# Performance work log

Measured on AMD Instinct MI355X. Metric: run time of the kernel, lower is better.

## Reference

```python
import jax, jax.numpy as jnp
import numpy as np

D_MODEL = 2048
N_HEAD = 32
N_KV_HEAD = 8
N_REP = N_HEAD // N_KV_HEAD
D_K = D_MODEL // N_HEAD
THETA = 10000.0
B, S = 2, 1024


def setup_inputs() -> dict:
    key = jax.random.key(0)
    ks = jax.random.split(key, 9)
    sd = 1.0 / np.sqrt(D_MODEL)
    return {
        "x": jax.random.normal(ks[0], (B, S, D_MODEL), jnp.float32),
        "Wq": jax.random.normal(ks[1], (D_MODEL, D_MODEL), jnp.float32) * sd,
        "bq": jax.random.normal(ks[2], (D_MODEL,), jnp.float32) * 0.02,
        "Wk": jax.random.normal(ks[3], (D_MODEL, N_KV_HEAD * D_K), jnp.float32) * sd,
        "bk": jax.random.normal(ks[4], (N_KV_HEAD * D_K,), jnp.float32) * 0.02,
        "Wv": jax.random.normal(ks[5], (D_MODEL, N_KV_HEAD * D_K), jnp.float32) * sd,
        "bv": jax.random.normal(ks[6], (N_KV_HEAD * D_K,), jnp.float32) * 0.02,
        "Wo": jax.random.normal(ks[7], (D_MODEL, D_MODEL), jnp.float32) * sd,
        "bo": jax.random.normal(ks[8], (D_MODEL,), jnp.float32) * 0.02,
    }


def _apply_rope(t, pos):
    # t: [b, h, s, d_k], pos: [s]
    half = D_K // 2
    inv_freq = 1.0 / (THETA ** (jnp.arange(half, dtype=jnp.float32) * 2.0 / D_K))
    ang = pos[:, None].astype(jnp.float32) * inv_freq[None, :]  # [s, half]
    cos = jnp.cos(ang)[None, None]  # [1,1,s,half]
    sin = jnp.sin(ang)[None, None]
    te = t[..., 0::2]
    to = t[..., 1::2]
    re = te * cos - to * sin
    ro = te * sin + to * cos
    return jnp.stack([re, ro], axis=-1).reshape(t.shape)


def reference(x, Wq, bq, Wk, bk, Wv, bv, Wo, bo):
    b, s, _ = x.shape
    q = (x @ Wq + bq).reshape(b, s, N_HEAD, D_K).transpose(0, 2, 1, 3)
    k = (x @ Wk + bk).reshape(b, s, N_KV_HEAD, D_K).transpose(0, 2, 1, 3)
    v = (x @ Wv + bv).reshape(b, s, N_KV_HEAD, D_K).transpose(0, 2, 1, 3)
    pos = jnp.arange(s)
    q = _apply_rope(q, pos)
    k = _apply_rope(k, pos)
    # GQA head repeat: [b, n_kv, s, d] -> [b, n_head, s, d]
    k = jnp.repeat(k, N_REP, axis=1)
    v = jnp.repeat(v, N_REP, axis=1)
    scores = jnp.einsum('bhnd,bhmd->bhnm', q, k) / jnp.sqrt(jnp.float32(D_K))
    mask = jnp.tril(jnp.ones((s, s), dtype=bool))
    scores = jnp.where(mask[None, None], scores, jnp.float32(-jnp.inf))
    probs = jax.nn.softmax(scores, axis=-1)
    out = jnp.einsum('bhnm,bhmd->bhnd', probs, v)
    out = out.transpose(0, 2, 1, 3).reshape(b, s, D_MODEL)
    return out @ Wo + bo
```

## Files before the change

### kernel.cpp

```cpp
#include <hip/hip_runtime.h>
#include <hip/hip_bf16.h>

#define D_MODEL 2048
#define N_HEAD 32
#define N_KV_HEAD 8
#define N_REP 4
#define D_K 64
#define S_LEN 1024
#define B_SZ 2
#define M_ROWS (B_SZ * S_LEN)
#define KV_DIM (N_KV_HEAD * D_K)
#define QKV_N 3072
#define KOFF 2048
#define VOFF 2560
#define LOG2E 1.44269504088896f

typedef __attribute__((ext_vector_type(8))) short short8;
typedef __attribute__((ext_vector_type(4))) float f32x4;

#define EXP2F(x) __builtin_amdgcn_exp2f(x)

__device__ inline unsigned short f2bf(float f) {
    union { float f; unsigned int u; } x{f};
    unsigned int r = x.u + 0x7fffu + ((x.u >> 16) & 1u);
    return (unsigned short)(r >> 16);
}
__device__ inline float bf2f(unsigned short b) {
    union { unsigned int u; float f; } x; x.u = ((unsigned int)b) << 16; return x.f;
}
__device__ inline void store_c(float* p, float v) { *p = v; }
__device__ inline void store_c(unsigned short* p, float v) { *p = f2bf(v); }

__device__ inline void load_lds16(const unsigned short* g, unsigned short* l) {
    __builtin_amdgcn_global_load_lds(
        (const __attribute__((address_space(1))) unsigned int*)g,
        (__attribute__((address_space(3))) unsigned int*)l, 16, 0, 0);
}

__global__ __launch_bounds__(256) void wprep_kernel(
        const float* __restrict__ Wq_, const float* __restrict__ Wk_,
        const float* __restrict__ Wv_, const float* __restrict__ Wo_,
        unsigned short* __restrict__ WtQKV, unsigned short* __restrict__ WtO) {
    const float* src; unsigned short* dst; int N;
    switch (blockIdx.z) {
        case 0: src = Wq_; dst = WtQKV; N = D_MODEL; break;
        case 1: src = Wk_; dst = WtQKV + (size_t)KOFF * D_MODEL; N = KV_DIM; break;
        case 2: src = Wv_; dst = WtQKV + (size_t)VOFF * D_MODEL; N = KV_DIM; break;
        default: src = Wo_; dst = WtO; N = D_MODEL; break;
    }
    int n0 = blockIdx.x * 64;
    if (n0 >= N) return;
    int k0 = blockIdx.y * 64;
    int t = threadIdx.x;
    int n = n0 + (t >> 2);
    int ks = k0 + (t & 3) * 16;
    unsigned int pk[8];
#pragma unroll
    for (int i = 0; i < 8; i++) {
        float a = src[(size_t)(ks + 2 * i) * N + n];
        float b = src[(size_t)(ks + 2 * i + 1) * N + n];
        pk[i] = (unsigned int)f2bf(a) | ((unsigned int)f2bf(b) << 16);
    }
    uint4* d = (uint4*)&dst[(size_t)n * D_MODEL + ks];
    d[0] = make_uint4(pk[0], pk[1], pk[2], pk[3]);
    d[1] = make_uint4(pk[4], pk[5], pk[6], pk[7]);
}

__global__ void cast_bf_kernel(const float* __restrict__ src,
                               unsigned short* __restrict__ dst, int n4) {
    int idx = blockIdx.x * blockDim.x + threadIdx.x;
    if (idx >= n4) return;
    float4 v = ((const float4*)src)[idx];
    unsigned int lo = (unsigned int)f2bf(v.x) | ((unsigned int)f2bf(v.y) << 16);
    unsigned int hi = (unsigned int)f2bf(v.z) | ((unsigned int)f2bf(v.w) << 16);
    ((uint2*)dst)[idx] = make_uint2(lo, hi);
}

__global__ void concat_bias_kernel(const float* __restrict__ bq, const float* __restrict__ bk,
                                   const float* __restrict__ bv, float* __restrict__ dst) {
    int i = blockIdx.x * blockDim.x + threadIdx.x;
    if (i >= QKV_N) return;
    dst[i] = (i < KOFF) ? bq[i] : (i < VOFF) ? bk[i - KOFF] : bv[i - VOFF];
}

template <typename TC>
__global__ __launch_bounds__(256) void gemm_bf16_kernel(
        const unsigned short* __restrict__ A,
        const unsigned short* __restrict__ Bt,
        const float* __restrict__ bias,
        TC* __restrict__ C, int M, int N, int K) {
    __shared__ unsigned short As[128 * 64];
    __shared__ unsigned short Bs[64 * 64];
    const int tid = threadIdx.x, lane = tid & 63;
    const int w = tid >> 6, wm = w >> 1, wn = w & 1;
    const int quad = lane >> 4, lr = lane & 15;
    const int bm = blockIdx.y * 128, bn = blockIdx.x * 64;

    f32x4 acc[4][2];
#pragma unroll
    for (int i = 0; i < 4; i++)
#pragma unroll
        for (int j = 0; j < 2; j++) acc[i][j] = (f32x4){0.f, 0.f, 0.f, 0.f};

    for (int k0 = 0; k0 < K; k0 += 64) {
        __syncthreads();
#pragma unroll
        for (int it = 0; it < 4; it++) {
            int slot = it * 256 + tid;
            int row = slot >> 3;
            int qc = (slot & 7) ^ (row & 7);
            load_lds16(A + (size_t)(bm + row) * K + k0 + qc * 8, &As[slot * 8]);
        }
#pragma unroll
        for (int it = 0; it < 2; it++) {
            int slot = it * 256 + tid;
            int row = slot >> 3;
            int qc = (slot & 7) ^ (row & 7);
            load_lds16(Bt + (size_t)(bn + row) * K + k0 + qc * 8, &Bs[slot * 8]);
        }
        __syncthreads();
#pragma unroll
        for (int ks = 0; ks < 2; ks++) {
            short8 af[4], bf[2];
#pragma unroll
            for (int i = 0; i < 4; i++) {
                int row = wm * 64 + i * 16 + lr;
                af[i] = *(const short8*)&As[(row * 8 + ((ks * 4 + quad) ^ (lr & 7))) * 8];
            }
#pragma unroll
            for (int j = 0; j < 2; j++) {
                int row = wn * 32 + j * 16 + lr;
                bf[j] = *(const short8*)&Bs[(row * 8 + ((ks * 4 + quad) ^ (lr & 7))) * 8];
            }
#pragma unroll
            for (int i = 0; i < 4; i++)
#pragma unroll
                for (int j = 0; j < 2; j++)
                    acc[i][j] = __builtin_amdgcn_mfma_f32_16x16x32_bf16(af[i], bf[j], acc[i][j], 0, 0, 0);
        }
    }
#pragma unroll
    for (int i = 0; i < 4; i++) {
#pragma unroll
        for (int j = 0; j < 2; j++) {
            int col = bn + wn * 32 + j * 16 + lr;
            int row0 = bm + wm * 64 + i * 16 + quad * 4;
            float bj = bias[col];
#pragma unroll
            for (int r = 0; r < 4; r++)
                store_c(&C[(size_t)(row0 + r) * N + col], acc[i][j][r] + bj);
        }
    }
}

__global__ void rope_bf_kernel(unsigned short* __restrict__ t) {
    const int QI = M_ROWS * N_HEAD * 32;
    const int TOT = QI + M_ROWS * N_KV_HEAD * 32;
    int idx = blockIdx.x * blockDim.x + threadIdx.x;
    if (idx >= TOT) return;
    int col_off, n_heads;
    float scale;
    if (idx < QI) { col_off = 0; n_heads = N_HEAD; scale = 0.125f * LOG2E; }
    else { idx -= QI; col_off = KOFF; n_heads = N_KV_HEAD; scale = 1.0f; }
    int i = idx & 31;
    int hh = (idx >> 5) % n_heads;
    int r = idx / (32 * n_heads);
    int s = r % S_LEN;
    float inv_freq = EXP2F((float)i * -0.41524101186f);
    float ang = (float)s * inv_freq;
    float c = __cosf(ang), sn = __sinf(ang);
    unsigned short* p = t + (size_t)r * QKV_N + col_off + hh * D_K + 2 * i;
    float te = bf2f(p[0]), to = bf2f(p[1]);
    p[0] = f2bf((te * c - to * sn) * scale);
    p[1] = f2bf((te * sn + to * c) * scale);
}

#define AST 72
__device__ __forceinline__ void attn_tile(
        int w, int quad, int lr, bool diag,
        const unsigned short* Ks, const unsigned short* Vt, unsigned short* Ps,
        const short8* aq, f32x4* oacc, float* mrow, float* lrow) {
    f32x4 s[4];
#pragma unroll
    for (int cf = 0; cf < 4; cf++) s[cf] = (f32x4){0.f, 0.f, 0.f, 0.f};
#pragma unroll
    for (int ks = 0; ks < 2; ks++) {
#pragma unroll
        for (int cf = 0; cf < 4; cf++) {
            short8 bk = *(const short8*)&Ks[(cf * 16 + lr) * AST + ks * 32 + quad * 8];
            s[cf] = __builtin_amdgcn_mfma_f32_16x16x32_bf16(aq[ks], bk, s[cf], 0, 0, 0);
        }
    }
    if (diag) {
#pragma unroll
        for (int cf = 0; cf < 4; cf++) {
            int key = cf * 16 + lr;
#pragma unroll
            for (int r = 0; r < 4; r++)
                if (key > w * 16 + quad * 4 + r) s[cf][r] = -1e30f;
        }
    }
    float corr[4];
#pragma unroll
    for (int r = 0; r < 4; r++) {
        float rm = fmaxf(fmaxf(s[0][r], s[1][r]), fmaxf(s[2][r], s[3][r]));
        rm = fmaxf(rm, __shfl_xor(rm, 1));
        rm = fmaxf(rm, __shfl_xor(rm, 2));
        rm = fmaxf(rm, __shfl_xor(rm, 4));
        rm = fmaxf(rm, __shfl_xor(rm, 8));
        float mn = fmaxf(mrow[r], rm);
        corr[r] = EXP2F(mrow[r] - mn);
        mrow[r] = mn;
        float rs = 0.f;
#pragma unroll
        for (int cf = 0; cf < 4; cf++) {
            float p = EXP2F(s[cf][r] - mn);
            union { float f; unsigned int u; } px{p};
            px.u &= 0xFFFF0000u;
            Ps[(w * 16 + quad * 4 + r) * AST + cf * 16 + lr] =
                (unsigned short)(px.u >> 16);
            rs += px.f;
        }
        rs += __shfl_xor(rs, 1);
        rs += __shfl_xor(rs, 2);
        rs += __shfl_xor(rs, 4);
        rs += __shfl_xor(rs, 8);
        lrow[r] = lrow[r] * corr[r] + rs;
    }
#pragma unroll
    for (int cf = 0; cf < 4; cf++)
#pragma unroll
        for (int r = 0; r < 4; r++) oacc[cf][r] *= corr[r];
#pragma unroll
    for (int ks = 0; ks < 2; ks++) {
        short8 ap = *(const short8*)&Ps[(w * 16 + lr) * AST + ks * 32 + quad * 8];
#pragma unroll
        for (int cf = 0; cf < 4; cf++) {
            short8 bv = *(const short8*)&Vt[(cf * 16 + lr) * AST + ks * 32 + quad * 8];
            oacc[cf] = __builtin_amdgcn_mfma_f32_16x16x32_bf16(ap, bv, oacc[cf], 0, 0, 0);
        }
    }
}

__global__ __launch_bounds__(256) void attn_mfma_kernel(
        const unsigned short* __restrict__ qkv,
        unsigned short* __restrict__ obf) {
    __shared__ unsigned short Ks[64 * AST];
    __shared__ unsigned short Vt[64 * AST];
    __shared__ unsigned short Ps[64 * AST];
    const int tid = threadIdx.x;
    const int w = tid >> 6, lane = tid & 63;
    const int lr = lane & 15, quad = lane >> 4;
    const int h = blockIdx.y, b = blockIdx.z;
    const int kvh = h >> 2;
    const unsigned short* kb = qkv + (size_t)(b * S_LEN) * QKV_N + KOFF + kvh * D_K;
    const unsigned short* vb = qkv + (size_t)(b * S_LEN) * QKV_N + VOFF + kvh * D_K;

    const int qt = 15 - (int)blockIdx.x;
    const int q0 = qt * 64;

    short8 aq[2];
    {
        const unsigned short* qp = qkv + (size_t)(b * S_LEN + q0 + w * 16 + lr) * QKV_N
                                   + h * D_K + quad * 8;
        aq[0] = *(const short8*)qp;
        aq[1] = *(const short8*)(qp + 32);
    }
    f32x4 oacc[4];
#pragma unroll
    for (int cf = 0; cf < 4; cf++) oacc[cf] = (f32x4){0.f, 0.f, 0.f, 0.f};
    float mrow[4] = {-1e30f, -1e30f, -1e30f, -1e30f};
    float lrow[4] = {0.f, 0.f, 0.f, 0.f};

    for (int t = 0; t <= qt; t++) {
        const int j0 = t * 64;
        __syncthreads();
#pragma unroll
        for (int it = 0; it < 2; it++) {
            int f = it * 256 + tid;
            int key = f >> 3, d8 = (f & 7) * 8;
            *(uint4*)&Ks[key * AST + d8] =
                *(const uint4*)(kb + (size_t)(j0 + key) * QKV_N + d8);
        }
        {
            int kp = tid & 31, dg = tid >> 5;
            unsigned short ta[8], tb[8];
            *(uint4*)ta = *(const uint4*)(vb + (size_t)(j0 + 2 * kp) * QKV_N + dg * 8);
            *(uint4*)tb = *(const uint4*)(vb + (size_t)(j0 + 2 * kp + 1) * QKV_N + dg * 8);
#pragma unroll
            for (int i = 0; i < 8; i++) {
                unsigned int pk = (unsigned int)ta[i] | ((unsigned int)tb[i] << 16);
                *(unsigned int*)&Vt[(dg * 8 + i) * AST + 2 * kp] = pk;
            }
        }
        __syncthreads();
        attn_tile(w, quad, lr, t == qt, Ks, Vt, Ps, aq, oacc, mrow, lrow);
    }
#pragma unroll
    for (int r = 0; r < 4; r++) {
        float inv = 1.f / lrow[r];
        int row = b * S_LEN + q0 + w * 16 + quad * 4 + r;
#pragma unroll
        for (int cf = 0; cf < 4; cf++)
            obf[(size_t)row * D_MODEL + h * D_K + cf * 16 + lr] = f2bf(oacc[cf][r] * inv);
    }
}

extern "C" void kernel_launch(void* const* d_in, const int* in_sizes, int n_in,
                              void* d_out, int out_size, void* d_ws, size_t ws_size,
                              hipStream_t stream) {
    const float* x  = (const float*)d_in[0];
    const float* Wq = (const float*)d_in[1];
    const float* bq = (const float*)d_in[2];
    const float* Wk = (const float*)d_in[3];
    const float* bk = (const float*)d_in[4];
    const float* Wv = (const float*)d_in[5];
    const float* bv = (const float*)d_in[6];
    const float* Wo = (const float*)d_in[7];
    const float* bo = (const float*)d_in[8];
    float* out = (float*)d_out;

    unsigned short* xbf   = (unsigned short*)d_ws;
    unsigned short* WtQKV = xbf + (size_t)M_ROWS * D_MODEL;
    unsigned short* WtO   = WtQKV + (size_t)QKV_N * D_MODEL;
    unsigned short* qkv   = WtO + (size_t)D_MODEL * D_MODEL;
    float* bias_qkv       = (float*)(qkv + (size_t)M_ROWS * QKV_N);
    unsigned short* obf   = xbf;

    dim3 gb(256);

    cast_bf_kernel<<<(M_ROWS * D_MODEL / 4 + 255) / 256, gb, 0, stream>>>(x, xbf, M_ROWS * D_MODEL / 4);
    wprep_kernel<<<dim3(32, 32, 4), gb, 0, stream>>>(Wq, Wk, Wv, Wo, WtQKV, WtO);
    concat_bias_kernel<<<(QKV_N + 255) / 256, gb, 0, stream>>>(bq, bk, bv, bias_qkv);
    gemm_bf16_kernel<unsigned short><<<dim3(QKV_N / 64, M_ROWS / 128), gb, 0, stream>>>(
        xbf, WtQKV, bias_qkv, qkv, M_ROWS, QKV_N, D_MODEL);
    rope_bf_kernel<<<(M_ROWS * (N_HEAD + N_KV_HEAD) * 32 + 255) / 256, gb, 0, stream>>>(qkv);
    attn_mfma_kernel<<<dim3(16, N_HEAD, B_SZ), gb, 0, stream>>>(qkv, obf);
    gemm_bf16_kernel<float><<<dim3(D_MODEL / 64, M_ROWS / 128), gb, 0, stream>>>(
        obf, WtO, bo, out, M_ROWS, D_MODEL, D_MODEL);
}
```

Baseline: 249.2 us.

## Pair causal query tiles per block and register-prefetch next K/V tile

Each attention block now handles two query tiles, qt and 15-qt, so every block does the same amount of causal work. The K/V tiles loaded into shared memory are reused by both query tiles, which halves K/V global loads. The next K/V tile is issued to registers while the current tile is being computed. The grid shrinks from 1024 to 512 blocks and each thread holds more registers, which may lower occupancy and parallelism on a large GPU.

```diff
diff --git a/kernel.cpp b/kernel.cpp
--- a/kernel.cpp
+++ b/kernel.cpp
@@ -176,6 +176,33 @@
 }
 
 #define AST 72
+struct Pre { uint4 k0, k1, v0, v1; };
+
+__device__ __forceinline__ void issue_pre(const unsigned short* kb,
+                                          const unsigned short* vb,
+                                          int j0, int tid, Pre& p) {
+    int f0 = tid, f1 = tid + 256;
+    p.k0 = *(const uint4*)(kb + (size_t)(j0 + (f0 >> 3)) * QKV_N + (f0 & 7) * 8);
+    p.k1 = *(const uint4*)(kb + (size_t)(j0 + (f1 >> 3)) * QKV_N + (f1 & 7) * 8);
+    int kp = tid & 31, dg = tid >> 5;
+    p.v0 = *(const uint4*)(vb + (size_t)(j0 + 2 * kp) * QKV_N + dg * 8);
+    p.v1 = *(const uint4*)(vb + (size_t)(j0 + 2 * kp + 1) * QKV_N + dg * 8);
+}
+__device__ __forceinline__ void commit_pre(unsigned short* Ks, unsigned short* Vt,
+                                           int tid, const Pre& p) {
+    int f0 = tid, f1 = tid + 256;
+    *(uint4*)&Ks[(f0 >> 3) * AST + (f0 & 7) * 8] = p.k0;
+    *(uint4*)&Ks[(f1 >> 3) * AST + (f1 & 7) * 8] = p.k1;
+    int kp = tid & 31, dg = tid >> 5;
+    const unsigned short* ta = (const unsigned short*)&p.v0;
+    const unsigned short* tb = (const unsigned short*)&p.v1;
+#pragma unroll
+    for (int i = 0; i < 8; i++) {
+        unsigned int pk = (unsigned int)ta[i] | ((unsigned int)tb[i] << 16);
+        *(unsigned int*)&Vt[(dg * 8 + i) * AST + 2 * kp] = pk;
+    }
+}
+
 __device__ __forceinline__ void attn_tile(
         int w, int quad, int lr, bool diag,
         const unsigned short* Ks, const unsigned short* Vt, unsigned short* Ps,
@@ -256,53 +283,50 @@
     const unsigned short* kb = qkv + (size_t)(b * S_LEN) * QKV_N + KOFF + kvh * D_K;
     const unsigned short* vb = qkv + (size_t)(b * S_LEN) * QKV_N + VOFF + kvh * D_K;
 
-    const int qt = 15 - (int)blockIdx.x;
-    const int q0 = qt * 64;
-
-    short8 aq[2];
+    const int qtA = blockIdx.x;
+    const int qtB = 15 - qtA;
+    const int ntA = qtA + 1, ntB = qtB + 1;
+
+    short8 aqA[2], aqB[2];
     {
-        const unsigned short* qp = qkv + (size_t)(b * S_LEN + q0 + w * 16 + lr) * QKV_N
+        const unsigned short* qp = qkv + (size_t)(b * S_LEN + qtA * 64 + w * 16 + lr) * QKV_N
                                    + h * D_K + quad * 8;
-        aq[0] = *(const short8*)qp;
-        aq[1] = *(const short8*)(qp + 32);
-    }
-    f32x4 oacc[4];
-#pragma unroll
-    for (int cf = 0; cf < 4; cf++) oacc[cf] = (f32x4){0.f, 0.f, 0.f, 0.f};
-    float mrow[4] = {-1e30f, -1e30f, -1e30f, -1e30f};
-    float lrow[4] = {0.f, 0.f, 0.f, 0.f};
-
-    for (int t = 0; t <= qt; t++) {
-        const int j0 = t * 64;
+        aqA[0] = *(const short8*)qp;
+        aqA[1] = *(const short8*)(qp + 32);
+        qp = qkv + (size_t)(b * S_LEN + qtB * 64 + w * 16 + lr) * QKV_N + h * D_K + quad * 8;
+        aqB[0] = *(const short8*)qp;
+        aqB[1] = *(const short8*)(qp + 32);
+    }
+    f32x4 oaccA[4], oaccB[4];
+#pragma unroll
+    for (int cf = 0; cf < 4; cf++) {
+        oaccA[cf] = (f32x4){0.f, 0.f, 0.f, 0.f};
+        oaccB[cf] = (f32x4){0.f, 0.f, 0.f, 0.f};
+    }
+    float mA[4] = {-1e30f, -1e30f, -1e30f, -1e30f}, lA[4] = {0.f, 0.f, 0.f, 0.f};
+    float mB[4] = {-1e30f, -1e30f, -1e30f, -1e30f}, lB[4] = {0.f, 0.f, 0.f, 0.f};
+
+    Pre pre;
+    issue_pre(kb, vb, 0, tid, pre);
+    for (int t = 0; t < ntB; t++) {
         __syncthreads();
-#pragma unroll
-        for (int it = 0; it < 2; it++) {
-            int f = it * 256 + tid;
-            int key = f >> 3, d8 = (f & 7) * 8;
-            *(uint4*)&Ks[key * AST + d8] =
-                *(const uint4*)(kb + (size_t)(j0 + key) * QKV_N + d8);
-        }
-        {
-            int kp = tid & 31, dg = tid >> 5;
-            unsigned short ta[8], tb[8];
-            *(uint4*)ta = *(const uint4*)(vb + (size_t)(j0 + 2 * kp) * QKV_N + dg * 8);
-            *(uint4*)tb = *(const uint4*)(vb + (size_t)(j0 + 2 * kp + 1) * QKV_N + dg * 8);
-#pragma unroll
-            for (int i = 0; i < 8; i++) {
-                unsigned int pk = (unsigned int)ta[i] | ((unsigned int)tb[i] << 16);
-                *(unsigned int*)&Vt[(dg * 8 + i) * AST + 2 * kp] = pk;
-            }
-        }
+        commit_pre(Ks, Vt, tid, pre);
         __syncthreads();
-        attn_tile(w, quad, lr, t == qt, Ks, Vt, Ps, aq, oacc, mrow, lrow);
+        if (t + 1 < ntB) issue_pre(kb, vb, (t + 1) * 64, tid, pre);
+        if (t < ntA)
+            attn_tile(w, quad, lr, t == qtA, Ks, Vt, Ps, aqA, oaccA, mA, lA);
+        attn_tile(w, quad, lr, t == qtB, Ks, Vt, Ps, aqB, oaccB, mB, lB);
     }
 #pragma unroll
     for (int r = 0; r < 4; r++) {
-        float inv = 1.f / lrow[r];
-        int row = b * S_LEN + q0 + w * 16 + quad * 4 + r;
-#pragma unroll
-        for (int cf = 0; cf < 4; cf++)
-            obf[(size_t)row * D_MODEL + h * D_K + cf * 16 + lr] = f2bf(oacc[cf][r] * inv);
+        float invA = 1.f / lA[r], invB = 1.f / lB[r];
+        int rowA = b * S_LEN + qtA * 64 + w * 16 + quad * 4 + r;
+        int rowB = b * S_LEN + qtB * 64 + w * 16 + quad * 4 + r;
+#pragma unroll
+        for (int cf = 0; cf < 4; cf++) {
+            obf[(size_t)rowA * D_MODEL + h * D_K + cf * 16 + lr] = f2bf(oaccA[cf][r] * invA);
+            obf[(size_t)rowB * D_MODEL + h * D_K + cf * 16 + lr] = f2bf(oaccB[cf][r] * invB);
+        }
     }
 }
 
@@ -335,7 +359,7 @@
     gemm_bf16_kernel<unsigned short><<<dim3(QKV_N / 64, M_ROWS / 128), gb, 0, stream>>>(
         xbf, WtQKV, bias_qkv, qkv, M_ROWS, QKV_N, D_MODEL);
     rope_bf_kernel<<<(M_ROWS * (N_HEAD + N_KV_HEAD) * 32 + 255) / 256, gb, 0, stream>>>(qkv);
-    attn_mfma_kernel<<<dim3(16, N_HEAD, B_SZ), gb, 0, stream>>>(qkv, obf);
+    attn_mfma_kernel<<<dim3(8, N_HEAD, B_SZ), gb, 0, stream>>>(qkv, obf);
     gemm_bf16_kernel<float><<<dim3(D_MODEL / 64, M_ROWS / 128), gb, 0, stream>>>(
         obf, WtO, bo, out, M_ROWS, D_MODEL, D_MODEL);
 }
```

Measured after the change: 232.8 us. 6.6% less time.

## Split long causal query tiles across two blocks with a combine kernel

Applied to the files above, without the earlier changes.

The attention grid grows from 16 to 24 blocks per head. Each of the 8 longest query tiles is split into two KV-range halves, and each half writes an unnormalized bf16 partial output plus its row max and sum to the workspace, reusing the QKV weight buffer. A new combine kernel merges the two halves with the softmax rescaling. The goal is to balance the triangular causal workload and shorten the critical path. The cost is an extra launch, extra global traffic, and bf16 rounding of the partial outputs.

```diff
diff --git a/kernel.cpp b/kernel.cpp
--- a/kernel.cpp
+++ b/kernel.cpp
@@ -244,7 +244,9 @@
 
 __global__ __launch_bounds__(256) void attn_mfma_kernel(
         const unsigned short* __restrict__ qkv,
-        unsigned short* __restrict__ obf) {
+        unsigned short* __restrict__ obf,
+        unsigned short* __restrict__ Po,
+        float* __restrict__ Pm, float* __restrict__ Pl) {
     __shared__ unsigned short Ks[64 * AST];
     __shared__ unsigned short Vt[64 * AST];
     __shared__ unsigned short Ps[64 * AST];
@@ -256,7 +258,19 @@
     const unsigned short* kb = qkv + (size_t)(b * S_LEN) * QKV_N + KOFF + kvh * D_K;
     const unsigned short* vb = qkv + (size_t)(b * S_LEN) * QKV_N + VOFF + kvh * D_K;
 
-    const int qt = 15 - (int)blockIdx.x;
+    const int gx = blockIdx.x;
+    int qt, sp, t0, t1;
+    if (gx < 16) {
+        qt = 15 - (gx >> 1);
+        sp = gx & 1;
+        int n = qt + 1, h0 = (n + 1) >> 1;
+        t0 = sp ? h0 : 0;
+        t1 = sp ? n : h0;
+    } else {
+        qt = 23 - gx;
+        sp = -1;
+        t0 = 0; t1 = qt + 1;
+    }
     const int q0 = qt * 64;
 
     short8 aq[2];
@@ -272,7 +286,7 @@
     float mrow[4] = {-1e30f, -1e30f, -1e30f, -1e30f};
     float lrow[4] = {0.f, 0.f, 0.f, 0.f};
 
-    for (int t = 0; t <= qt; t++) {
+    for (int t = t0; t < t1; t++) {
         const int j0 = t * 64;
         __syncthreads();
 #pragma unroll
@@ -296,14 +310,52 @@
         __syncthreads();
         attn_tile(w, quad, lr, t == qt, Ks, Vt, Ps, aq, oacc, mrow, lrow);
     }
-#pragma unroll
-    for (int r = 0; r < 4; r++) {
-        float inv = 1.f / lrow[r];
-        int row = b * S_LEN + q0 + w * 16 + quad * 4 + r;
-#pragma unroll
-        for (int cf = 0; cf < 4; cf++)
-            obf[(size_t)row * D_MODEL + h * D_K + cf * 16 + lr] = f2bf(oacc[cf][r] * inv);
-    }
+
+    if (sp < 0) {
+#pragma unroll
+        for (int r = 0; r < 4; r++) {
+            float inv = 1.f / lrow[r];
+            int row = b * S_LEN + q0 + w * 16 + quad * 4 + r;
+#pragma unroll
+            for (int cf = 0; cf < 4; cf++)
+                obf[(size_t)row * D_MODEL + h * D_K + cf * 16 + lr] = f2bf(oacc[cf][r] * inv);
+        }
+    } else {
+        int pidx = ((b * N_HEAD + h) * 8 + (qt - 8)) * 2 + sp;
+#pragma unroll
+        for (int r = 0; r < 4; r++) {
+            int row = w * 16 + quad * 4 + r;
+            if (lr == 0) {
+                Pm[(size_t)pidx * 64 + row] = mrow[r];
+                Pl[(size_t)pidx * 64 + row] = lrow[r];
+            }
+#pragma unroll
+            for (int cf = 0; cf < 4; cf++)
+                Po[(size_t)pidx * 4096 + row * 64 + cf * 16 + lr] = f2bf(oacc[cf][r]);
+        }
+    }
+}
+
+__global__ __launch_bounds__(256) void attn_combine_kernel(
+        const unsigned short* __restrict__ Po, const float* __restrict__ Pm,
+        const float* __restrict__ Pl, unsigned short* __restrict__ obf) {
+    int qt8 = blockIdx.x, h = blockIdx.y, b = blockIdx.z;
+    int tid = threadIdx.x;
+    int row = tid >> 2;
+    int d0 = (tid & 3) * 16;
+    int pb = ((b * N_HEAD + h) * 8 + qt8) * 2;
+    float m0 = Pm[(size_t)pb * 64 + row],       m1 = Pm[(size_t)(pb + 1) * 64 + row];
+    float l0 = Pl[(size_t)pb * 64 + row],       l1 = Pl[(size_t)(pb + 1) * 64 + row];
+    float M = fmaxf(m0, m1);
+    float w0 = EXP2F(m0 - M), w1 = EXP2F(m1 - M);
+    float inv = 1.f / (w0 * l0 + w1 * l1);
+    const unsigned short* O0 = Po + (size_t)pb * 4096 + row * 64 + d0;
+    const unsigned short* O1 = Po + (size_t)(pb + 1) * 4096 + row * 64 + d0;
+    int grow = b * S_LEN + (8 + qt8) * 64 + row;
+    unsigned short* dst = obf + (size_t)grow * D_MODEL + h * D_K + d0;
+#pragma unroll
+    for (int i = 0; i < 16; i++)
+        dst[i] = f2bf((w0 * bf2f(O0[i]) + w1 * bf2f(O1[i])) * inv);
 }
 
 extern "C" void kernel_launch(void* const* d_in, const int* in_sizes, int n_in,
@@ -326,6 +378,9 @@
     unsigned short* qkv   = WtO + (size_t)D_MODEL * D_MODEL;
     float* bias_qkv       = (float*)(qkv + (size_t)M_ROWS * QKV_N);
     unsigned short* obf   = xbf;
+    unsigned short* Po = WtQKV;
+    float* Pm = (float*)(WtQKV + (size_t)1024 * 4096);
+    float* Pl = Pm + (size_t)1024 * 64;
 
     dim3 gb(256);
 
@@ -335,7 +390,8 @@
     gemm_bf16_kernel<unsigned short><<<dim3(QKV_N / 64, M_ROWS / 128), gb, 0, stream>>>(
         xbf, WtQKV, bias_qkv, qkv, M_ROWS, QKV_N, D_MODEL);
     rope_bf_kernel<<<(M_ROWS * (N_HEAD + N_KV_HEAD) * 32 + 255) / 256, gb, 0, stream>>>(qkv);
-    attn_mfma_kernel<<<dim3(16, N_HEAD, B_SZ), gb, 0, stream>>>(qkv, obf);
+    attn_mfma_kernel<<<dim3(24, N_HEAD, B_SZ), gb, 0, stream>>>(qkv, obf, Po, Pm, Pl);
+    attn_combine_kernel<<<dim3(8, N_HEAD, B_SZ), gb, 0, stream>>>(Po, Pm, Pl, obf);
     gemm_bf16_kernel<float><<<dim3(D_MODEL / 64, M_ROWS / 128), gb, 0, stream>>>(
         obf, WtO, bo, out, M_ROWS, D_MODEL, D_MODEL);
 }
```

New measurement: 242.0 us. 1.03x faster.
